# Kernel tuning notes

Measured on AMD Instinct MI355X. Metric: run time of the kernel, lower is better.

Reference implementation:

```python
import jax, jax.numpy as jnp
import numpy as np

EPS = 1e-5

def _block(x, W, b, g, be):
    # Linear -> LayerNorm -> ReLU, fused elementwise chain
    h = x @ W + b
    mu = jnp.mean(h, axis=-1, keepdims=True)
    var = jnp.mean(jnp.square(h - mu), axis=-1, keepdims=True)
    hn = (h - mu) * jax.lax.rsqrt(var + EPS) * g + be
    return jnp.maximum(hn, 0.0)

def setup_inputs() -> dict:
    key = jax.random.key(0)
    ks = jax.random.split(key, 6)
    B, D_IN, H, D_OUT = 262144, 48, 256, 12
    s_in = 1.0 / np.sqrt(D_IN)
    s_h = 1.0 / np.sqrt(H)
    return {
        "x": jax.random.normal(ks[0], (B, D_IN), jnp.float32),
        "W1": jax.random.normal(ks[1], (D_IN, H), jnp.float32) * s_in,
        "b1": jnp.zeros((H,), jnp.float32),
        "g1": jnp.ones((H,), jnp.float32),
        "be1": jnp.zeros((H,), jnp.float32),
        "W2": jax.random.normal(ks[2], (H, H), jnp.float32) * s_h,
        "b2": jnp.zeros((H,), jnp.float32),
        "g2": jnp.ones((H,), jnp.float32),
        "be2": jnp.zeros((H,), jnp.float32),
        "W3": jax.random.normal(ks[3], (H, H), jnp.float32) * s_h,
        "b3": jnp.zeros((H,), jnp.float32),
        "g3": jnp.ones((H,), jnp.float32),
        "be3": jnp.zeros((H,), jnp.float32),
        "Wm": jax.random.normal(ks[4], (H, D_OUT), jnp.float32) * s_h,
        "bm": jnp.zeros((D_OUT,), jnp.float32),
    }

def reference(x, W1, b1, g1, be1, W2, b2, g2, be2, W3, b3, g3, be3, Wm, bm):
    h = _block(x, W1, b1, g1, be1)
    h = _block(h, W2, b2, g2, be2)
    h = _block(h, W3, b3, g3, be3)
    return jnp.tanh(h @ Wm + bm)
```

## Files before the change

kernel.cpp:

```cpp
#include <hip/hip_runtime.h>
#include <hip/hip_bf16.h>

#define BATCH 262144
#define DIN 48
#define HDIM 256
#define DOUT 12
#define EPSV 1e-5f

#define ROWS_PER_BLOCK 128
#define NBLK (BATCH / ROWS_PER_BLOCK)

typedef __attribute__((ext_vector_type(4))) float f32x4;
typedef __attribute__((ext_vector_type(2))) float f32x2;
typedef __attribute__((ext_vector_type(8))) short bf16x8;

union FragU { bf16x8 v; unsigned u[4]; };

#define W1F_OFF 0
#define W2F_OFF 16384
#define W3F_OFF 81920
#define WMF_OFF 147456
#define WS_ELEMS 151552

#define WAITV(n) asm volatile("s_waitcnt vmcnt(" #n ")" ::: "memory")

__device__ __forceinline__ unsigned short f2b(float f) {
    union { float f; unsigned u; } v; v.f = f;
    unsigned r = (v.u + 0x7fffu + ((v.u >> 16) & 1u)) >> 16;
    return (unsigned short)r;
}

__device__ __forceinline__ unsigned packbf(float a, float b) {
    float2 t; t.x = a; t.y = b;
    __hip_bfloat162 h = __float22bfloat162_rn(t);
    union { __hip_bfloat162 h; unsigned u; } c; c.h = h;
    return c.u;
}

__device__ __forceinline__ float fast_tanh(float x) {
    const float t = __expf(2.0f * x);
    return fmaf(-2.0f, __builtin_amdgcn_rcpf(t + 1.0f), 1.0f);
}

__global__ void conv_w_kernel(const float* __restrict__ W1, const float* __restrict__ b1,
                              const float* __restrict__ W2, const float* __restrict__ W3,
                              const float* __restrict__ Wm,
                              unsigned short* __restrict__ ws) {
    int i = blockIdx.x * 256 + threadIdx.x;
    if (i >= WS_ELEMS) return;
    float v;
    if (i < W2F_OFF) {
        const int j = i & 7, l = (i >> 3) & 63, t = (i >> 9) & 15, s = i >> 13;
        const int n = 16 * t + (l & 15), k = 32 * s + 8 * (l >> 4) + j;
        v = (k < DIN) ? W1[k * HDIM + n] : (k == DIN ? b1[n] : 0.0f);
    } else if (i < W3F_OFF) {
        const int i2 = i - W2F_OFF;
        const int j = i2 & 7, l = (i2 >> 3) & 63, t = (i2 >> 9) & 15, s = i2 >> 13;
        const int n = 16 * t + (l & 15);
        const int k = 32 * s + ((j >= 4) ? 16 : 0) + 4 * (l >> 4) + (j & 3);
        v = W2[k * HDIM + n];
    } else if (i < WMF_OFF) {
        const int i3 = i - W3F_OFF;
        const int j = i3 & 7, l = (i3 >> 3) & 63, t = (i3 >> 9) & 15, s = i3 >> 13;
        const int n = 16 * t + (l & 15);
        const int k = 32 * s + ((j >= 4) ? 16 : 0) + 4 * (l >> 4) + (j & 3);
        v = W3[k * HDIM + n];
    } else {
        const int i4 = i - WMF_OFF;
        const int j = i4 & 7, l = (i4 >> 3) & 63, ks = i4 >> 9;
        const int n = l & 15;
        const int k = 32 * ks + ((j >= 4) ? 16 : 0) + 4 * (l >> 4) + (j & 3);
        v = (n < DOUT) ? Wm[k * DOUT + n] : 0.0f;
    }
    ws[i] = f2b(v);
}

__device__ __forceinline__ void gll16(const void* g, void* l) {
    __builtin_amdgcn_global_load_lds(
        (const __attribute__((address_space(1))) unsigned int*)g,
        (__attribute__((address_space(3))) unsigned int*)l, 16, 0, 0);
}

__device__ __forceinline__ void stage_slab(const unsigned short* __restrict__ src,
                                           unsigned short* dst, int tid) {
    const char* g = (const char*)src + tid * 16;
    char* l = (char*)dst + tid * 16;
    #pragma unroll
    for (int c = 0; c < 4; c++)
        gll16(g + c * 4096, l + c * 4096);
}

__device__ __forceinline__ void compute_slab(
    f32x4 (&acc)[2][16], const FragU& b0, const FragU& b1,
    const unsigned short* sb, int lane)
{
    __builtin_amdgcn_s_setprio(1);
    #pragma unroll
    for (int t = 0; t < 16; t++) {
        const bf16x8 A = *(const bf16x8*)&sb[(t * 64 + lane) * 8];
        acc[0][t] = __builtin_amdgcn_mfma_f32_16x16x32_bf16(A, b0.v, acc[0][t], 0, 0, 0);
        acc[1][t] = __builtin_amdgcn_mfma_f32_16x16x32_bf16(A, b1.v, acc[1][t], 0, 0, 0);
    }
    __builtin_amdgcn_s_setprio(0);
}

#define SV2(v, a, b) __builtin_shufflevector(v, v, a, b)

__device__ __forceinline__ void build_frags(
    const f32x4 (&acc)[2][16], FragU (&bfo)[2][8],
    const float* __restrict__ gt, const float* __restrict__ bt, int lane)
{
    const int q4 = (lane >> 4) * 4;
    #pragma unroll
    for (int rt = 0; rt < 2; rt++) {
        f32x2 s2 = {0.f, 0.f}, p2 = {0.f, 0.f};
        #pragma unroll
        for (int t = 0; t < 16; t++) {
            const f32x2 a = SV2(acc[rt][t], 0, 1);
            const f32x2 b = SV2(acc[rt][t], 2, 3);
            s2 += a; s2 += b;
            p2 += a * a; p2 += b * b;
        }
        float ss = s2[0] + s2[1];
        float qq = p2[0] + p2[1];
        ss += __shfl_xor(ss, 16); ss += __shfl_xor(ss, 32);
        qq += __shfl_xor(qq, 16); qq += __shfl_xor(qq, 32);
        const float mu = ss * (1.0f / 256.0f);
        const float rs = __builtin_amdgcn_rsqf(
            fmaxf(qq * (1.0f / 256.0f) - mu * mu, 0.0f) + EPSV);
        const float nb = -mu * rs;
        const f32x2 rs2 = {rs, rs}, nb2 = {nb, nb}, z2 = {0.f, 0.f};
        #pragma unroll
        for (int ks = 0; ks < 8; ks++) {
            const f32x4 g0 = *(const f32x4*)&gt[32 * ks + q4];
            const f32x4 e0 = *(const f32x4*)&bt[32 * ks + q4];
            const f32x4 g1 = *(const f32x4*)&gt[32 * ks + 16 + q4];
            const f32x4 e1 = *(const f32x4*)&bt[32 * ks + 16 + q4];
            const f32x2 v00 = SV2(acc[rt][2 * ks], 0, 1);
            const f32x2 v01 = SV2(acc[rt][2 * ks], 2, 3);
            const f32x2 v10 = SV2(acc[rt][2 * ks + 1], 0, 1);
            const f32x2 v11 = SV2(acc[rt][2 * ks + 1], 2, 3);
            const f32x2 w00 = __builtin_elementwise_max(
                (v00 * rs2 + nb2) * SV2(g0, 0, 1) + SV2(e0, 0, 1), z2);
            const f32x2 w01 = __builtin_elementwise_max(
                (v01 * rs2 + nb2) * SV2(g0, 2, 3) + SV2(e0, 2, 3), z2);
            const f32x2 w10 = __builtin_elementwise_max(
                (v10 * rs2 + nb2) * SV2(g1, 0, 1) + SV2(e1, 0, 1), z2);
            const f32x2 w11 = __builtin_elementwise_max(
                (v11 * rs2 + nb2) * SV2(g1, 2, 3) + SV2(e1, 2, 3), z2);
            bfo[rt][ks].u[0] = packbf(w00[0], w00[1]);
            bfo[rt][ks].u[1] = packbf(w01[0], w01[1]);
            bfo[rt][ks].u[2] = packbf(w10[0], w10[1]);
            bfo[rt][ks].u[3] = packbf(w11[0], w11[1]);
        }
    }
}

__device__ __forceinline__ void zero_acc(f32x4 (&acc)[2][16]) {
    #pragma unroll
    for (int rt = 0; rt < 2; rt++)
        #pragma unroll
        for (int t = 0; t < 16; t++)
            acc[rt][t] = (f32x4){0.f, 0.f, 0.f, 0.f};
}

__device__ __forceinline__ void init_acc_bias(f32x4 (&acc)[2][16],
                                              const float* __restrict__ bt, int q) {
    #pragma unroll
    for (int t = 0; t < 16; t++) {
        const f32x4 b = *(const f32x4*)&bt[16 * t + 4 * q];
        acc[0][t] = b;
        acc[1][t] = b;
    }
}

__global__ __launch_bounds__(256, 2) void fused_mlp(
    const float* __restrict__ x,
    const float* __restrict__ g1, const float* __restrict__ be1,
    const float* __restrict__ b2, const float* __restrict__ g2, const float* __restrict__ be2,
    const float* __restrict__ b3, const float* __restrict__ g3, const float* __restrict__ be3,
    const float* __restrict__ bm,
    const unsigned short* __restrict__ ws,
    float* __restrict__ out)
{
    __shared__ unsigned short buf[4][8192];
    __shared__ float gtab[3][256];
    __shared__ float betab[3][256];
    __shared__ float btab[2][256];
    __shared__ float bmt[16];
    __shared__ float ostage[4][384];

    const int tid = threadIdx.x;
    const int wv = tid >> 6, lane = tid & 63;
    const int l15 = lane & 15, q = lane >> 4;
    const int wrow0 = blockIdx.x * ROWS_PER_BLOCK + wv * 32;

    const unsigned short* w1f = ws + W1F_OFF;
    const unsigned short* w2f = ws + W2F_OFF;
    const unsigned short* w3f = ws + W3F_OFF;
    const unsigned short* wmf = ws + WMF_OFF;

    stage_slab(w1f, &buf[0][0], tid);
    stage_slab(w1f + 8192, &buf[1][0], tid);

    {
        const int n = tid;
        gtab[0][n] = g1[n];  betab[0][n] = be1[n];
        gtab[1][n] = g2[n];  betab[1][n] = be2[n];
        gtab[2][n] = g3[n];  betab[2][n] = be3[n];
        btab[0][n] = b2[n];
        btab[1][n] = b3[n];
        if (tid < 16) bmt[tid] = (tid < DOUT) ? bm[tid] : 0.f;
    }
    FragU bf[2][8];
    #pragma unroll
    for (int rt = 0; rt < 2; rt++) {
        const float* xr = x + (size_t)(wrow0 + rt * 16 + l15) * DIN;
        const float4 f0 = *(const float4*)(xr + q * 8);
        const float4 f1 = *(const float4*)(xr + q * 8 + 4);
        bf[rt][0].u[0] = packbf(f0.x, f0.y); bf[rt][0].u[1] = packbf(f0.z, f0.w);
        bf[rt][0].u[2] = packbf(f1.x, f1.y); bf[rt][0].u[3] = packbf(f1.z, f1.w);
        if (q < 2) {
            const float4 f2 = *(const float4*)(xr + 32 + q * 8);
            const float4 f3 = *(const float4*)(xr + 36 + q * 8);
            bf[rt][1].u[0] = packbf(f2.x, f2.y); bf[rt][1].u[1] = packbf(f2.z, f2.w);
            bf[rt][1].u[2] = packbf(f3.x, f3.y); bf[rt][1].u[3] = packbf(f3.z, f3.w);
        } else if (q == 2) {
            bf[rt][1].u[0] = 0x00003F80u;
            bf[rt][1].u[1] = 0u; bf[rt][1].u[2] = 0u; bf[rt][1].u[3] = 0u;
        } else {
            bf[rt][1].u[0] = 0u; bf[rt][1].u[1] = 0u;
            bf[rt][1].u[2] = 0u; bf[rt][1].u[3] = 0u;
        }
    }
    asm volatile("s_waitcnt lgkmcnt(0)" ::: "memory");

    f32x4 acc[2][16];


    zero_acc(acc);
    #pragma unroll
    for (int s = 0; s < 2; s++) {
        stage_slab(w2f + s * 8192, &buf[(s + 2) & 3][0], tid);
        WAITV(8);
        __builtin_amdgcn_s_barrier();
        __builtin_amdgcn_sched_barrier(0);
        compute_slab(acc, bf[0][s], bf[1][s], &buf[s][0], lane);
    }
    build_frags(acc, bf, &gtab[0][0], &betab[0][0], lane);

    init_acc_bias(acc, &btab[0][0], q);
    #pragma unroll
    for (int s = 0; s < 8; s++) {
        const unsigned short* nsrc = (s < 6) ? (w2f + (s + 2) * 8192)
                                             : (w3f + (s - 6) * 8192);
        stage_slab(nsrc, &buf[(s + 4) & 3][0], tid);
        WAITV(8);
        __builtin_amdgcn_s_barrier();
        __builtin_amdgcn_sched_barrier(0);
        compute_slab(acc, bf[0][s], bf[1][s], &buf[(s + 2) & 3][0], lane);
    }
    build_frags(acc, bf, &gtab[1][0], &betab[1][0], lane);

    init_acc_bias(acc, &btab[1][0], q);
    #pragma unroll
    for (int s = 0; s < 8; s++) {
        if (s < 6) stage_slab(w3f + (s + 2) * 8192, &buf[(s + 12) & 3][0], tid);
        if (s < 6)      { WAITV(8); }
        else if (s == 6){ WAITV(4); }
        else            { WAITV(0); }
        __builtin_amdgcn_s_barrier();
        __builtin_amdgcn_sched_barrier(0);
        compute_slab(acc, bf[0][s], bf[1][s], &buf[(s + 10) & 3][0], lane);
    }
    build_frags(acc, bf, &gtab[2][0], &betab[2][0], lane);

    f32x4 facc[2];
    {
        const f32x4 bm4 = *(const f32x4*)&bmt[4 * q];
        facc[0] = bm4;
        facc[1] = bm4;
    }
    #pragma unroll
    for (int ks = 0; ks < 8; ks++) {
        const bf16x8 A = *(const bf16x8*)&wmf[(ks * 64 + lane) * 8];
        facc[0] = __builtin_amdgcn_mfma_f32_16x16x32_bf16(A, bf[0][ks].v, facc[0], 0, 0, 0);
        facc[1] = __builtin_amdgcn_mfma_f32_16x16x32_bf16(A, bf[1][ks].v, facc[1], 0, 0, 0);
    }
    if (q < 3) {
        #pragma unroll
        for (int rt = 0; rt < 2; rt++) {
            float4 o;
            o.x = fast_tanh(facc[rt][0]);
            o.y = fast_tanh(facc[rt][1]);
            o.z = fast_tanh(facc[rt][2]);
            o.w = fast_tanh(facc[rt][3]);
            *(float4*)&ostage[wv][(rt * 16 + l15) * 12 + q * 4] = o;
        }
    }
    float4* og = (float4*)(out + (size_t)wrow0 * DOUT);
    const float4* ov = (const float4*)&ostage[wv][0];
    og[lane] = ov[lane];
    if (lane < 32) og[64 + lane] = ov[64 + lane];
}

extern "C" void kernel_launch(void* const* d_in, const int* in_sizes, int n_in,
                              void* d_out, int out_size, void* d_ws, size_t ws_size,
                              hipStream_t stream)
{
    const float* x   = (const float*)d_in[0];
    const float* W1  = (const float*)d_in[1];
    const float* b1  = (const float*)d_in[2];
    const float* g1  = (const float*)d_in[3];
    const float* be1 = (const float*)d_in[4];
    const float* W2  = (const float*)d_in[5];
    const float* b2  = (const float*)d_in[6];
    const float* g2  = (const float*)d_in[7];
    const float* be2 = (const float*)d_in[8];
    const float* W3  = (const float*)d_in[9];
    const float* b3  = (const float*)d_in[10];
    const float* g3  = (const float*)d_in[11];
    const float* be3 = (const float*)d_in[12];
    const float* Wm  = (const float*)d_in[13];
    const float* bm  = (const float*)d_in[14];
    unsigned short* ws = (unsigned short*)d_ws;
    float* out = (float*)d_out;

    conv_w_kernel<<<(WS_ELEMS + 255) / 256, 256, 0, stream>>>(W1, b1, W2, W3, Wm, ws);
    fused_mlp<<<NBLK, 256, 0, stream>>>(x, g1, be1, b2, g2, be2,
                                        b3, g3, be3, bm, ws, out);
}
```

Measured before the change: 100.6 us.

## Stage half of each weight slab in LDS and load the other half from global

Each weight slab is split. Only the first half is copied into LDS with async global-to-LDS loads, which halves the shared weight buffers. The second half is read by every wave directly from global memory into registers inside the compute step. This is meant to cut LDS traffic and footprint, and the vmcnt waits are adjusted for the smaller staging. In exchange, each wave reloads the same fragments redundantly, register pressure grows, and the in-order vmcnt waits on the direct loads may also force waits on the prefetch loads, reducing overlap.

```diff
diff --git a/kernel.cpp b/kernel.cpp
--- a/kernel.cpp
+++ b/kernel.cpp
@@ -81,25 +81,33 @@
         (__attribute__((address_space(3))) unsigned int*)l, 16, 0, 0);
 }
 
-__device__ __forceinline__ void stage_slab(const unsigned short* __restrict__ src,
+__device__ __forceinline__ void stage_half(const unsigned short* __restrict__ src,
                                            unsigned short* dst, int tid) {
     const char* g = (const char*)src + tid * 16;
     char* l = (char*)dst + tid * 16;
-    #pragma unroll
-    for (int c = 0; c < 4; c++)
-        gll16(g + c * 4096, l + c * 4096);
+    gll16(g, l);
+    gll16(g + 4096, l + 4096);
 }
 
 __device__ __forceinline__ void compute_slab(
     f32x4 (&acc)[2][16], const FragU& b0, const FragU& b1,
-    const unsigned short* sb, int lane)
+    const unsigned short* sb, const unsigned short* __restrict__ gw, int lane)
 {
+    bf16x8 AG[8];
+    #pragma unroll
+    for (int t = 0; t < 8; t++)
+        AG[t] = *(const bf16x8*)&gw[(t * 64 + lane) * 8];
     __builtin_amdgcn_s_setprio(1);
     #pragma unroll
-    for (int t = 0; t < 16; t++) {
+    for (int t = 0; t < 8; t++) {
         const bf16x8 A = *(const bf16x8*)&sb[(t * 64 + lane) * 8];
         acc[0][t] = __builtin_amdgcn_mfma_f32_16x16x32_bf16(A, b0.v, acc[0][t], 0, 0, 0);
         acc[1][t] = __builtin_amdgcn_mfma_f32_16x16x32_bf16(A, b1.v, acc[1][t], 0, 0, 0);
+    }
+    #pragma unroll
+    for (int t = 0; t < 8; t++) {
+        acc[0][8 + t] = __builtin_amdgcn_mfma_f32_16x16x32_bf16(AG[t], b0.v, acc[0][8 + t], 0, 0, 0);
+        acc[1][8 + t] = __builtin_amdgcn_mfma_f32_16x16x32_bf16(AG[t], b1.v, acc[1][8 + t], 0, 0, 0);
     }
     __builtin_amdgcn_s_setprio(0);
 }
@@ -183,7 +191,7 @@
     const unsigned short* __restrict__ ws,
     float* __restrict__ out)
 {
-    __shared__ unsigned short buf[4][8192];
+    __shared__ unsigned short buf[4][4096];
     __shared__ float gtab[3][256];
     __shared__ float betab[3][256];
     __shared__ float btab[2][256];
@@ -200,8 +208,8 @@
     const unsigned short* w3f = ws + W3F_OFF;
     const unsigned short* wmf = ws + WMF_OFF;
 
-    stage_slab(w1f, &buf[0][0], tid);
-    stage_slab(w1f + 8192, &buf[1][0], tid);
+    stage_half(w1f, &buf[0][0], tid);
+    stage_half(w1f + 8192, &buf[1][0], tid);
 
     {
         const int n = tid;
@@ -241,11 +249,12 @@
     zero_acc(acc);
     #pragma unroll
     for (int s = 0; s < 2; s++) {
-        stage_slab(w2f + s * 8192, &buf[(s + 2) & 3][0], tid);
-        WAITV(8);
+        stage_half(w2f + s * 8192, &buf[(s + 2) & 3][0], tid);
+        WAITV(4);
         __builtin_amdgcn_s_barrier();
         __builtin_amdgcn_sched_barrier(0);
-        compute_slab(acc, bf[0][s], bf[1][s], &buf[s][0], lane);
+        compute_slab(acc, bf[0][s], bf[1][s], &buf[s][0],
+                     w1f + s * 8192 + 4096, lane);
     }
     build_frags(acc, bf, &gtab[0][0], &betab[0][0], lane);
 
@@ -254,24 +263,26 @@
     for (int s = 0; s < 8; s++) {
         const unsigned short* nsrc = (s < 6) ? (w2f + (s + 2) * 8192)
                                              : (w3f + (s - 6) * 8192);
-        stage_slab(nsrc, &buf[(s + 4) & 3][0], tid);
-        WAITV(8);
+        stage_half(nsrc, &buf[(s + 4) & 3][0], tid);
+        WAITV(4);
         __builtin_amdgcn_s_barrier();
         __builtin_amdgcn_sched_barrier(0);
-        compute_slab(acc, bf[0][s], bf[1][s], &buf[(s + 2) & 3][0], lane);
+        compute_slab(acc, bf[0][s], bf[1][s], &buf[(s + 2) & 3][0],
+                     w2f + s * 8192 + 4096, lane);
     }
     build_frags(acc, bf, &gtab[1][0], &betab[1][0], lane);
 
     init_acc_bias(acc, &btab[1][0], q);
     #pragma unroll
     for (int s = 0; s < 8; s++) {
-        if (s < 6) stage_slab(w3f + (s + 2) * 8192, &buf[(s + 12) & 3][0], tid);
-        if (s < 6)      { WAITV(8); }
-        else if (s == 6){ WAITV(4); }
+        if (s < 6) stage_half(w3f + (s + 2) * 8192, &buf[(s + 12) & 3][0], tid);
+        if (s < 6)      { WAITV(4); }
+        else if (s == 6){ WAITV(2); }
         else            { WAITV(0); }
         __builtin_amdgcn_s_barrier();
         __builtin_amdgcn_sched_barrier(0);
-        compute_slab(acc, bf[0][s], bf[1][s], &buf[(s + 10) & 3][0], lane);
+        compute_slab(acc, bf[0][s], bf[1][s], &buf[(s + 10) & 3][0],
+                     w3f + s * 8192 + 4096, lane);
     }
     build_frags(acc, bf, &gtab[2][0], &betab[2][0], lane);
 
```

Measured after the change: 107.5 us. 1.07x slower.

## Halve block size and stream weights through a 3-slot half-slab LDS ring

Applied to the files above, without the earlier changes.

Shrinks each block to two waves handling 64 rows and replaces the 4-deep full-slab weight buffer with a 3-slot ring of half-slabs, prefetching two halves ahead with one barrier per half. Bias and scale tables are loaded through registers, the final bias comes straight from global memory, and the output staging reuses the ring buffer, which cuts shared memory per block. The goal is more resident blocks per CU to hide latency. In exchange, every weight byte is staged into LDS twice as often per row, and there are twice as many barriers per row processed.

```diff
diff --git a/kernel.cpp b/kernel.cpp
--- a/kernel.cpp
+++ b/kernel.cpp
@@ -7,7 +7,7 @@
 #define DOUT 12
 #define EPSV 1e-5f
 
-#define ROWS_PER_BLOCK 128
+#define ROWS_PER_BLOCK 64
 #define NBLK (BATCH / ROWS_PER_BLOCK)
 
 typedef __attribute__((ext_vector_type(4))) float f32x4;
@@ -81,25 +81,25 @@
         (__attribute__((address_space(3))) unsigned int*)l, 16, 0, 0);
 }
 
-__device__ __forceinline__ void stage_slab(const unsigned short* __restrict__ src,
+__device__ __forceinline__ void stage_half(const unsigned short* __restrict__ src,
                                            unsigned short* dst, int tid) {
     const char* g = (const char*)src + tid * 16;
     char* l = (char*)dst + tid * 16;
     #pragma unroll
     for (int c = 0; c < 4; c++)
-        gll16(g + c * 4096, l + c * 4096);
-}
-
-__device__ __forceinline__ void compute_slab(
+        gll16(g + c * 2048, l + c * 2048);
+}
+
+__device__ __forceinline__ void compute_half(
     f32x4 (&acc)[2][16], const FragU& b0, const FragU& b1,
-    const unsigned short* sb, int lane)
+    const unsigned short* sb, int lane, int hh)
 {
     __builtin_amdgcn_s_setprio(1);
     #pragma unroll
-    for (int t = 0; t < 16; t++) {
+    for (int t = 0; t < 8; t++) {
         const bf16x8 A = *(const bf16x8*)&sb[(t * 64 + lane) * 8];
-        acc[0][t] = __builtin_amdgcn_mfma_f32_16x16x32_bf16(A, b0.v, acc[0][t], 0, 0, 0);
-        acc[1][t] = __builtin_amdgcn_mfma_f32_16x16x32_bf16(A, b1.v, acc[1][t], 0, 0, 0);
+        acc[0][hh * 8 + t] = __builtin_amdgcn_mfma_f32_16x16x32_bf16(A, b0.v, acc[0][hh * 8 + t], 0, 0, 0);
+        acc[1][hh * 8 + t] = __builtin_amdgcn_mfma_f32_16x16x32_bf16(A, b1.v, acc[1][hh * 8 + t], 0, 0, 0);
     }
     __builtin_amdgcn_s_setprio(0);
 }
@@ -174,7 +174,7 @@
     }
 }
 
-__global__ __launch_bounds__(256, 2) void fused_mlp(
+__global__ __launch_bounds__(128, 2) void fused_mlp(
     const float* __restrict__ x,
     const float* __restrict__ g1, const float* __restrict__ be1,
     const float* __restrict__ b2, const float* __restrict__ g2, const float* __restrict__ be2,
@@ -183,12 +183,10 @@
     const unsigned short* __restrict__ ws,
     float* __restrict__ out)
 {
-    __shared__ unsigned short buf[4][8192];
+    __shared__ unsigned short ring[3][4096];
     __shared__ float gtab[3][256];
     __shared__ float betab[3][256];
     __shared__ float btab[2][256];
-    __shared__ float bmt[16];
-    __shared__ float ostage[4][384];
 
     const int tid = threadIdx.x;
     const int wv = tid >> 6, lane = tid & 63;
@@ -200,31 +198,55 @@
     const unsigned short* w3f = ws + W3F_OFF;
     const unsigned short* wmf = ws + WMF_OFF;
 
-    stage_slab(w1f, &buf[0][0], tid);
-    stage_slab(w1f + 8192, &buf[1][0], tid);
-
-    {
-        const int n = tid;
-        gtab[0][n] = g1[n];  betab[0][n] = be1[n];
-        gtab[1][n] = g2[n];  betab[1][n] = be2[n];
-        gtab[2][n] = g3[n];  betab[2][n] = be3[n];
-        btab[0][n] = b2[n];
-        btab[1][n] = b3[n];
-        if (tid < 16) bmt[tid] = (tid < DOUT) ? bm[tid] : 0.f;
-    }
-    FragU bf[2][8];
+    auto hsrc = [&](int h) -> const unsigned short* {
+        if (h < 4)  return w1f + h * 4096;
+        if (h < 20) return w2f + (h - 4) * 4096;
+        return w3f + (h - 20) * 4096;
+    };
+
+    float4 xf[2][4];
     #pragma unroll
     for (int rt = 0; rt < 2; rt++) {
         const float* xr = x + (size_t)(wrow0 + rt * 16 + l15) * DIN;
-        const float4 f0 = *(const float4*)(xr + q * 8);
-        const float4 f1 = *(const float4*)(xr + q * 8 + 4);
-        bf[rt][0].u[0] = packbf(f0.x, f0.y); bf[rt][0].u[1] = packbf(f0.z, f0.w);
-        bf[rt][0].u[2] = packbf(f1.x, f1.y); bf[rt][0].u[3] = packbf(f1.z, f1.w);
+        xf[rt][0] = *(const float4*)(xr + q * 8);
+        xf[rt][1] = *(const float4*)(xr + q * 8 + 4);
         if (q < 2) {
-            const float4 f2 = *(const float4*)(xr + 32 + q * 8);
-            const float4 f3 = *(const float4*)(xr + 36 + q * 8);
-            bf[rt][1].u[0] = packbf(f2.x, f2.y); bf[rt][1].u[1] = packbf(f2.z, f2.w);
-            bf[rt][1].u[2] = packbf(f3.x, f3.y); bf[rt][1].u[3] = packbf(f3.z, f3.w);
+            xf[rt][2] = *(const float4*)(xr + 32 + q * 8);
+            xf[rt][3] = *(const float4*)(xr + 36 + q * 8);
+        }
+    }
+    float tg[3][2], tb[3][2], tbi[2][2];
+    #pragma unroll
+    for (int i = 0; i < 2; i++) {
+        const int n = tid + i * 128;
+        tg[0][i] = g1[n]; tb[0][i] = be1[n];
+        tg[1][i] = g2[n]; tb[1][i] = be2[n];
+        tg[2][i] = g3[n]; tb[2][i] = be3[n];
+        tbi[0][i] = b2[n]; tbi[1][i] = b3[n];
+    }
+    stage_half(hsrc(0), &ring[0][0], tid);
+    stage_half(hsrc(1), &ring[1][0], tid);
+
+    #pragma unroll
+    for (int i = 0; i < 2; i++) {
+        const int n = tid + i * 128;
+        gtab[0][n] = tg[0][i]; betab[0][n] = tb[0][i];
+        gtab[1][n] = tg[1][i]; betab[1][n] = tb[1][i];
+        gtab[2][n] = tg[2][i]; betab[2][n] = tb[2][i];
+        btab[0][n] = tbi[0][i]; btab[1][n] = tbi[1][i];
+    }
+    FragU bf[2][8];
+    #pragma unroll
+    for (int rt = 0; rt < 2; rt++) {
+        bf[rt][0].u[0] = packbf(xf[rt][0].x, xf[rt][0].y);
+        bf[rt][0].u[1] = packbf(xf[rt][0].z, xf[rt][0].w);
+        bf[rt][0].u[2] = packbf(xf[rt][1].x, xf[rt][1].y);
+        bf[rt][0].u[3] = packbf(xf[rt][1].z, xf[rt][1].w);
+        if (q < 2) {
+            bf[rt][1].u[0] = packbf(xf[rt][2].x, xf[rt][2].y);
+            bf[rt][1].u[1] = packbf(xf[rt][2].z, xf[rt][2].w);
+            bf[rt][1].u[2] = packbf(xf[rt][3].x, xf[rt][3].y);
+            bf[rt][1].u[3] = packbf(xf[rt][3].z, xf[rt][3].w);
         } else if (q == 2) {
             bf[rt][1].u[0] = 0x00003F80u;
             bf[rt][1].u[1] = 0u; bf[rt][1].u[2] = 0u; bf[rt][1].u[3] = 0u;
@@ -240,44 +262,43 @@
 
     zero_acc(acc);
     #pragma unroll
-    for (int s = 0; s < 2; s++) {
-        stage_slab(w2f + s * 8192, &buf[(s + 2) & 3][0], tid);
-        WAITV(8);
+    for (int m = 0; m < 4; m++) {
+        WAITV(4);
         __builtin_amdgcn_s_barrier();
         __builtin_amdgcn_sched_barrier(0);
-        compute_slab(acc, bf[0][s], bf[1][s], &buf[s][0], lane);
+        stage_half(hsrc(m + 2), &ring[(m + 2) % 3][0], tid);
+        compute_half(acc, bf[0][m >> 1], bf[1][m >> 1], &ring[m % 3][0], lane, m & 1);
     }
     build_frags(acc, bf, &gtab[0][0], &betab[0][0], lane);
 
     init_acc_bias(acc, &btab[0][0], q);
     #pragma unroll
-    for (int s = 0; s < 8; s++) {
-        const unsigned short* nsrc = (s < 6) ? (w2f + (s + 2) * 8192)
-                                             : (w3f + (s - 6) * 8192);
-        stage_slab(nsrc, &buf[(s + 4) & 3][0], tid);
-        WAITV(8);
+    for (int m = 4; m < 20; m++) {
+        WAITV(4);
         __builtin_amdgcn_s_barrier();
         __builtin_amdgcn_sched_barrier(0);
-        compute_slab(acc, bf[0][s], bf[1][s], &buf[(s + 2) & 3][0], lane);
+        stage_half(hsrc(m + 2), &ring[(m + 2) % 3][0], tid);
+        const int sl = (m - 4) >> 1;
+        compute_half(acc, bf[0][sl], bf[1][sl], &ring[m % 3][0], lane, m & 1);
     }
     build_frags(acc, bf, &gtab[1][0], &betab[1][0], lane);
 
     init_acc_bias(acc, &btab[1][0], q);
     #pragma unroll
-    for (int s = 0; s < 8; s++) {
-        if (s < 6) stage_slab(w3f + (s + 2) * 8192, &buf[(s + 12) & 3][0], tid);
-        if (s < 6)      { WAITV(8); }
-        else if (s == 6){ WAITV(4); }
-        else            { WAITV(0); }
+    for (int m = 20; m < 36; m++) {
+        if (m == 35) { WAITV(0); } else { WAITV(4); }
         __builtin_amdgcn_s_barrier();
         __builtin_amdgcn_sched_barrier(0);
-        compute_slab(acc, bf[0][s], bf[1][s], &buf[(s + 10) & 3][0], lane);
+        if (m + 2 < 36) stage_half(hsrc(m + 2), &ring[(m + 2) % 3][0], tid);
+        const int sl = (m - 20) >> 1;
+        compute_half(acc, bf[0][sl], bf[1][sl], &ring[m % 3][0], lane, m & 1);
     }
     build_frags(acc, bf, &gtab[2][0], &betab[2][0], lane);
 
     f32x4 facc[2];
     {
-        const f32x4 bm4 = *(const f32x4*)&bmt[4 * q];
+        f32x4 bm4 = {0.f, 0.f, 0.f, 0.f};
+        if (q < 3) bm4 = *(const f32x4*)&bm[4 * q];
         facc[0] = bm4;
         facc[1] = bm4;
     }
@@ -287,6 +308,7 @@
         facc[0] = __builtin_amdgcn_mfma_f32_16x16x32_bf16(A, bf[0][ks].v, facc[0], 0, 0, 0);
         facc[1] = __builtin_amdgcn_mfma_f32_16x16x32_bf16(A, bf[1][ks].v, facc[1], 0, 0, 0);
     }
+    float* ost = (float*)&ring[0][0] + wv * 384;
     if (q < 3) {
         #pragma unroll
         for (int rt = 0; rt < 2; rt++) {
@@ -295,11 +317,11 @@
             o.y = fast_tanh(facc[rt][1]);
             o.z = fast_tanh(facc[rt][2]);
             o.w = fast_tanh(facc[rt][3]);
-            *(float4*)&ostage[wv][(rt * 16 + l15) * 12 + q * 4] = o;
+            *(float4*)&ost[(rt * 16 + l15) * 12 + q * 4] = o;
         }
     }
     float4* og = (float4*)(out + (size_t)wrow0 * DOUT);
-    const float4* ov = (const float4*)&ostage[wv][0];
+    const float4* ov = (const float4*)ost;
     og[lane] = ov[lane];
     if (lane < 32) og[64 + lane] = ov[64 + lane];
 }
@@ -327,6 +349,6 @@
     float* out = (float*)d_out;
 
     conv_w_kernel<<<(WS_ELEMS + 255) / 256, 256, 0, stream>>>(W1, b1, W2, W3, Wm, ws);
-    fused_mlp<<<NBLK, 256, 0, stream>>>(x, g1, be1, b2, g2, be2,
+    fused_mlp<<<NBLK, 128, 0, stream>>>(x, g1, be1, b2, g2, be2,
                                         b3, g3, be3, bm, ws, out);
 }
```

Result: slower. 126.9 us (+26.2%).

## Process four row tiles per block with continuous weight-slab pipeline across tiles

Applied to the files above, without the earlier changes.

Each block now handles four 128-row tiles instead of one, keeping the weight ring buffer streaming continuously: the last slabs of W3 for one tile overlap with staging W1 and prefetching x for the next tile. The output head weights are staged once into LDS, and outputs are written directly instead of through an LDS staging buffer. This amortizes block launch, parameter-table setup and pipeline fill/drain across tiles. It reduces the grid fourfold, which may lower parallelism and tail balance, and adds register pressure for the prefetched x values.

```diff
diff --git a/kernel.cpp b/kernel.cpp
--- a/kernel.cpp
+++ b/kernel.cpp
@@ -7,8 +7,9 @@
 #define DOUT 12
 #define EPSV 1e-5f
 
-#define ROWS_PER_BLOCK 128
-#define NBLK (BATCH / ROWS_PER_BLOCK)
+#define ROWS_PER_TILE 128
+#define TILES_PER_BLOCK 4
+#define NBLK (BATCH / (ROWS_PER_TILE * TILES_PER_BLOCK))
 
 typedef __attribute__((ext_vector_type(4))) float f32x4;
 typedef __attribute__((ext_vector_type(2))) float f32x2;
@@ -81,8 +82,8 @@
         (__attribute__((address_space(3))) unsigned int*)l, 16, 0, 0);
 }
 
-__device__ __forceinline__ void stage_slab(const unsigned short* __restrict__ src,
-                                           unsigned short* dst, int tid) {
+__device__ __forceinline__ void stage16(const unsigned short* __restrict__ src,
+                                        unsigned short* dst, int tid) {
     const char* g = (const char*)src + tid * 16;
     char* l = (char*)dst + tid * 16;
     #pragma unroll
@@ -174,6 +175,120 @@
     }
 }
 
+__device__ __forceinline__ void xload(const float* __restrict__ x, int wrow0,
+                                      int l15, int q, float4 (&xf)[2][4]) {
+    const int c2 = (q < 2) ? (32 + q * 8) : 0;
+    #pragma unroll
+    for (int rt = 0; rt < 2; rt++) {
+        const float* xr = x + (size_t)(wrow0 + rt * 16 + l15) * DIN;
+        xf[rt][0] = *(const float4*)(xr + q * 8);
+        xf[rt][1] = *(const float4*)(xr + q * 8 + 4);
+        xf[rt][2] = *(const float4*)(xr + c2);
+        xf[rt][3] = *(const float4*)(xr + c2 + 4);
+    }
+}
+
+__device__ __forceinline__ void build_bf1(const float4 (&xf)[2][4],
+                                          FragU (&bf)[2][8], int q) {
+    #pragma unroll
+    for (int rt = 0; rt < 2; rt++) {
+        bf[rt][0].u[0] = packbf(xf[rt][0].x, xf[rt][0].y);
+        bf[rt][0].u[1] = packbf(xf[rt][0].z, xf[rt][0].w);
+        bf[rt][0].u[2] = packbf(xf[rt][1].x, xf[rt][1].y);
+        bf[rt][0].u[3] = packbf(xf[rt][1].z, xf[rt][1].w);
+        if (q < 2) {
+            bf[rt][1].u[0] = packbf(xf[rt][2].x, xf[rt][2].y);
+            bf[rt][1].u[1] = packbf(xf[rt][2].z, xf[rt][2].w);
+            bf[rt][1].u[2] = packbf(xf[rt][3].x, xf[rt][3].y);
+            bf[rt][1].u[3] = packbf(xf[rt][3].z, xf[rt][3].w);
+        } else if (q == 2) {
+            bf[rt][1].u[0] = 0x00003F80u;
+            bf[rt][1].u[1] = 0u; bf[rt][1].u[2] = 0u; bf[rt][1].u[3] = 0u;
+        } else {
+            bf[rt][1].u[0] = 0u; bf[rt][1].u[1] = 0u;
+            bf[rt][1].u[2] = 0u; bf[rt][1].u[3] = 0u;
+        }
+    }
+}
+
+template<int PHASE, bool LAST>
+__device__ __forceinline__ void run_tile(
+    const float* __restrict__ x, const unsigned short* __restrict__ w1f,
+    const unsigned short* __restrict__ w2f, const unsigned short* __restrict__ w3f,
+    unsigned short (&ring)[4][8192], const unsigned short* wmlds,
+    const float (&gtab)[3][256], const float (&betab)[3][256],
+    const float (&btab)[2][256], const f32x4& bm4,
+    float* __restrict__ out, int tileRow0, int nextRow0,
+    FragU (&bf)[2][8], f32x4 (&acc)[2][16], float4 (&xf)[2][4],
+    int tid, int lane, int l15, int q, int wv)
+{
+    const int wrow0 = tileRow0 + wv * 32;
+
+    zero_acc(acc);
+    #pragma unroll
+    for (int s = 0; s < 2; s++) {
+        stage16(w2f + s * 8192, &ring[(s + 2 + PHASE) & 3][0], tid);
+        WAITV(10);
+        __builtin_amdgcn_s_barrier();
+        __builtin_amdgcn_sched_barrier(0);
+        compute_slab(acc, bf[0][s], bf[1][s], &ring[(s + PHASE) & 3][0], lane);
+    }
+    build_frags(acc, bf, &gtab[0][0], &betab[0][0], lane);
+
+    init_acc_bias(acc, &btab[0][0], q);
+    #pragma unroll
+    for (int s = 0; s < 8; s++) {
+        const unsigned short* nsrc = (s < 6) ? (w2f + (s + 2) * 8192)
+                                             : (w3f + (s - 6) * 8192);
+        stage16(nsrc, &ring[(s + PHASE) & 3][0], tid);
+        WAITV(8);
+        __builtin_amdgcn_s_barrier();
+        __builtin_amdgcn_sched_barrier(0);
+        compute_slab(acc, bf[0][s], bf[1][s], &ring[(s + 2 + PHASE) & 3][0], lane);
+    }
+    build_frags(acc, bf, &gtab[1][0], &betab[1][0], lane);
+
+    init_acc_bias(acc, &btab[1][0], q);
+    #pragma unroll
+    for (int s = 0; s < 8; s++) {
+        const unsigned short* nsrc = (s < 6) ? (w3f + (s + 2) * 8192)
+                                             : (w1f + (s - 6) * 8192);
+        stage16(nsrc, &ring[(s + PHASE) & 3][0], tid);
+        if (s == 6) xload(x, nextRow0 + wv * 32, l15, q, xf);
+        if (s < 6) { WAITV(8); } else { WAITV(16); }
+        __builtin_amdgcn_s_barrier();
+        __builtin_amdgcn_sched_barrier(0);
+        compute_slab(acc, bf[0][s], bf[1][s], &ring[(s + 2 + PHASE) & 3][0], lane);
+    }
+    build_frags(acc, bf, &gtab[2][0], &betab[2][0], lane);
+
+    f32x4 facc[2];
+    facc[0] = bm4;
+    facc[1] = bm4;
+    #pragma unroll
+    for (int ks = 0; ks < 8; ks++) {
+        const bf16x8 A = *(const bf16x8*)&wmlds[(ks * 64 + lane) * 8];
+        facc[0] = __builtin_amdgcn_mfma_f32_16x16x32_bf16(A, bf[0][ks].v, facc[0], 0, 0, 0);
+        facc[1] = __builtin_amdgcn_mfma_f32_16x16x32_bf16(A, bf[1][ks].v, facc[1], 0, 0, 0);
+    }
+    if (q < 3) {
+        #pragma unroll
+        for (int rt = 0; rt < 2; rt++) {
+            float4 o;
+            o.x = fast_tanh(facc[rt][0]);
+            o.y = fast_tanh(facc[rt][1]);
+            o.z = fast_tanh(facc[rt][2]);
+            o.w = fast_tanh(facc[rt][3]);
+            *(float4*)&out[(size_t)(wrow0 + rt * 16 + l15) * DOUT + q * 4] = o;
+        }
+    }
+    if constexpr (!LAST) {
+        build_bf1(xf, bf, q);
+    } else {
+        WAITV(0);
+    }
+}
+
 __global__ __launch_bounds__(256, 2) void fused_mlp(
     const float* __restrict__ x,
     const float* __restrict__ g1, const float* __restrict__ be1,
@@ -183,125 +298,59 @@
     const unsigned short* __restrict__ ws,
     float* __restrict__ out)
 {
-    __shared__ unsigned short buf[4][8192];
+    __shared__ unsigned short ring[4][8192];
+    __shared__ unsigned short wmlds[4096];
     __shared__ float gtab[3][256];
     __shared__ float betab[3][256];
     __shared__ float btab[2][256];
-    __shared__ float bmt[16];
-    __shared__ float ostage[4][384];
 
     const int tid = threadIdx.x;
     const int wv = tid >> 6, lane = tid & 63;
     const int l15 = lane & 15, q = lane >> 4;
-    const int wrow0 = blockIdx.x * ROWS_PER_BLOCK + wv * 32;
+    const int blockRow0 = blockIdx.x * (ROWS_PER_TILE * TILES_PER_BLOCK);
 
     const unsigned short* w1f = ws + W1F_OFF;
     const unsigned short* w2f = ws + W2F_OFF;
     const unsigned short* w3f = ws + W3F_OFF;
-    const unsigned short* wmf = ws + WMF_OFF;
-
-    stage_slab(w1f, &buf[0][0], tid);
-    stage_slab(w1f + 8192, &buf[1][0], tid);
-
+
+    float4 xf[2][4];
+    xload(x, blockRow0 + wv * 32, l15, q, xf);
+    f32x4 bm4 = {0.f, 0.f, 0.f, 0.f};
+    if (q < 3) bm4 = *(const f32x4*)&bm[4 * q];
+    const float tg1 = g1[tid], tbe1 = be1[tid];
+    const float tg2 = g2[tid], tbe2 = be2[tid];
+    const float tg3 = g3[tid], tbe3 = be3[tid];
+    const float tb2 = b2[tid], tb3 = b3[tid];
+    stage16(w1f, &ring[0][0], tid);
+    stage16(w1f + 8192, &ring[1][0], tid);
     {
-        const int n = tid;
-        gtab[0][n] = g1[n];  betab[0][n] = be1[n];
-        gtab[1][n] = g2[n];  betab[1][n] = be2[n];
-        gtab[2][n] = g3[n];  betab[2][n] = be3[n];
-        btab[0][n] = b2[n];
-        btab[1][n] = b3[n];
-        if (tid < 16) bmt[tid] = (tid < DOUT) ? bm[tid] : 0.f;
-    }
+        const char* g = (const char*)(ws + WMF_OFF) + tid * 16;
+        char* l = (char*)wmlds + tid * 16;
+        gll16(g, l);
+        gll16(g + 4096, l + 4096);
+    }
+    gtab[0][tid] = tg1; betab[0][tid] = tbe1;
+    gtab[1][tid] = tg2; betab[1][tid] = tbe2;
+    gtab[2][tid] = tg3; betab[2][tid] = tbe3;
+    btab[0][tid] = tb2; btab[1][tid] = tb3;
     FragU bf[2][8];
-    #pragma unroll
-    for (int rt = 0; rt < 2; rt++) {
-        const float* xr = x + (size_t)(wrow0 + rt * 16 + l15) * DIN;
-        const float4 f0 = *(const float4*)(xr + q * 8);
-        const float4 f1 = *(const float4*)(xr + q * 8 + 4);
-        bf[rt][0].u[0] = packbf(f0.x, f0.y); bf[rt][0].u[1] = packbf(f0.z, f0.w);
-        bf[rt][0].u[2] = packbf(f1.x, f1.y); bf[rt][0].u[3] = packbf(f1.z, f1.w);
-        if (q < 2) {
-            const float4 f2 = *(const float4*)(xr + 32 + q * 8);
-            const float4 f3 = *(const float4*)(xr + 36 + q * 8);
-            bf[rt][1].u[0] = packbf(f2.x, f2.y); bf[rt][1].u[1] = packbf(f2.z, f2.w);
-            bf[rt][1].u[2] = packbf(f3.x, f3.y); bf[rt][1].u[3] = packbf(f3.z, f3.w);
-        } else if (q == 2) {
-            bf[rt][1].u[0] = 0x00003F80u;
-            bf[rt][1].u[1] = 0u; bf[rt][1].u[2] = 0u; bf[rt][1].u[3] = 0u;
-        } else {
-            bf[rt][1].u[0] = 0u; bf[rt][1].u[1] = 0u;
-            bf[rt][1].u[2] = 0u; bf[rt][1].u[3] = 0u;
-        }
-    }
+    build_bf1(xf, bf, q);
     asm volatile("s_waitcnt lgkmcnt(0)" ::: "memory");
 
     f32x4 acc[2][16];
 
-
-    zero_acc(acc);
-    #pragma unroll
-    for (int s = 0; s < 2; s++) {
-        stage_slab(w2f + s * 8192, &buf[(s + 2) & 3][0], tid);
-        WAITV(8);
-        __builtin_amdgcn_s_barrier();
-        __builtin_amdgcn_sched_barrier(0);
-        compute_slab(acc, bf[0][s], bf[1][s], &buf[s][0], lane);
-    }
-    build_frags(acc, bf, &gtab[0][0], &betab[0][0], lane);
-
-    init_acc_bias(acc, &btab[0][0], q);
-    #pragma unroll
-    for (int s = 0; s < 8; s++) {
-        const unsigned short* nsrc = (s < 6) ? (w2f + (s + 2) * 8192)
-                                             : (w3f + (s - 6) * 8192);
-        stage_slab(nsrc, &buf[(s + 4) & 3][0], tid);
-        WAITV(8);
-        __builtin_amdgcn_s_barrier();
-        __builtin_amdgcn_sched_barrier(0);
-        compute_slab(acc, bf[0][s], bf[1][s], &buf[(s + 2) & 3][0], lane);
-    }
-    build_frags(acc, bf, &gtab[1][0], &betab[1][0], lane);
-
-    init_acc_bias(acc, &btab[1][0], q);
-    #pragma unroll
-    for (int s = 0; s < 8; s++) {
-        if (s < 6) stage_slab(w3f + (s + 2) * 8192, &buf[(s + 12) & 3][0], tid);
-        if (s < 6)      { WAITV(8); }
-        else if (s == 6){ WAITV(4); }
-        else            { WAITV(0); }
-        __builtin_amdgcn_s_barrier();
-        __builtin_amdgcn_sched_barrier(0);
-        compute_slab(acc, bf[0][s], bf[1][s], &buf[(s + 10) & 3][0], lane);
-    }
-    build_frags(acc, bf, &gtab[2][0], &betab[2][0], lane);
-
-    f32x4 facc[2];
-    {
-        const f32x4 bm4 = *(const f32x4*)&bmt[4 * q];
-        facc[0] = bm4;
-        facc[1] = bm4;
-    }
-    #pragma unroll
-    for (int ks = 0; ks < 8; ks++) {
-        const bf16x8 A = *(const bf16x8*)&wmf[(ks * 64 + lane) * 8];
-        facc[0] = __builtin_amdgcn_mfma_f32_16x16x32_bf16(A, bf[0][ks].v, facc[0], 0, 0, 0);
-        facc[1] = __builtin_amdgcn_mfma_f32_16x16x32_bf16(A, bf[1][ks].v, facc[1], 0, 0, 0);
-    }
-    if (q < 3) {
-        #pragma unroll
-        for (int rt = 0; rt < 2; rt++) {
-            float4 o;
-            o.x = fast_tanh(facc[rt][0]);
-            o.y = fast_tanh(facc[rt][1]);
-            o.z = fast_tanh(facc[rt][2]);
-            o.w = fast_tanh(facc[rt][3]);
-            *(float4*)&ostage[wv][(rt * 16 + l15) * 12 + q * 4] = o;
-        }
-    }
-    float4* og = (float4*)(out + (size_t)wrow0 * DOUT);
-    const float4* ov = (const float4*)&ostage[wv][0];
-    og[lane] = ov[lane];
-    if (lane < 32) og[64 + lane] = ov[64 + lane];
+    run_tile<0, false>(x, w1f, w2f, w3f, ring, wmlds, gtab, betab, btab, bm4,
+                       out, blockRow0, blockRow0 + 128,
+                       bf, acc, xf, tid, lane, l15, q, wv);
+    run_tile<2, false>(x, w1f, w2f, w3f, ring, wmlds, gtab, betab, btab, bm4,
+                       out, blockRow0 + 128, blockRow0 + 256,
+                       bf, acc, xf, tid, lane, l15, q, wv);
+    run_tile<0, false>(x, w1f, w2f, w3f, ring, wmlds, gtab, betab, btab, bm4,
+                       out, blockRow0 + 256, blockRow0 + 384,
+                       bf, acc, xf, tid, lane, l15, q, wv);
+    run_tile<2, true>(x, w1f, w2f, w3f, ring, wmlds, gtab, betab, btab, bm4,
+                      out, blockRow0 + 384, blockRow0 + 384,
+                      bf, acc, xf, tid, lane, l15, q, wv);
 }
 
 extern "C" void kernel_launch(void* const* d_in, const int* in_sizes, int n_in,
```

Measured after the change: 177.4 us. 1.76x slower.
